# Performance work log

Measured on AMD Instinct MI355X. Metric: run time of the kernel, lower is better.

The kernel has to match this reference:

```python
import math
import jax, jax.numpy as jnp
import numpy as np

NUM_BUCKETS = 32
MAX_DISTANCE = 128
HEADS = 16
D_MODEL = 1024
SEQ = 1024
BATCH = 4
SCALE = (D_MODEL // HEADS) ** -0.5  # applied ONLY to the relative-position bias, per the source


def _rel_pos_bucket_causal(seq_len):
    """Causal T5 relative-position bucket: ret[i, j] for query i, key j."""
    pos = jnp.arange(seq_len)
    # rel_pos = k - q ; n = -rel_pos = q - k, clamped at 0 (causal branch)
    n = jnp.maximum(pos[:, None] - pos[None, :], 0)
    max_exact = NUM_BUCKETS // 2  # 16
    # log-spaced buckets for large distances; guard n>=1 to avoid log(0)
    val_large = max_exact + (
        jnp.log(jnp.maximum(n, 1).astype(jnp.float32) / max_exact)
        / math.log(MAX_DISTANCE / max_exact)
        * (NUM_BUCKETS - max_exact)
    ).astype(jnp.int32)
    val_large = jnp.minimum(val_large, NUM_BUCKETS - 1)
    return jnp.where(n < max_exact, n, val_large)  # [i, j] int32


def setup_inputs() -> dict:
    key = jax.random.key(0)
    ks = jax.random.split(key, 6)
    s = 0.02
    return {
        "x": jax.random.normal(ks[0], (BATCH, SEQ, D_MODEL), jnp.float32),
        "Wq": jax.random.normal(ks[1], (D_MODEL, D_MODEL), jnp.float32) * s,
        "bq": jnp.zeros((D_MODEL,), jnp.float32),
        "Wk": jax.random.normal(ks[2], (D_MODEL, D_MODEL), jnp.float32) * s,
        "bk": jnp.zeros((D_MODEL,), jnp.float32),
        "Wv": jax.random.normal(ks[3], (D_MODEL, D_MODEL), jnp.float32) * s,
        "bv": jnp.zeros((D_MODEL,), jnp.float32),
        "Wo": jax.random.normal(ks[4], (D_MODEL, D_MODEL), jnp.float32) * s,
        "bo": jnp.zeros((D_MODEL,), jnp.float32),
        "rel_emb": jax.random.normal(ks[5], (NUM_BUCKETS, HEADS), jnp.float32) * s,
    }


def reference(x, Wq, bq, Wk, bk, Wv, bv, Wo, bo, rel_emb):
    b, n, d = x.shape
    h, hd = HEADS, d // HEADS
    # projections (torch Linear: x @ W^T + b)
    q = (x @ Wq.T + bq).reshape(b, n, h, hd).transpose(0, 2, 1, 3)  # bhnd
    k = (x @ Wk.T + bk).reshape(b, n, h, hd).transpose(0, 2, 1, 3)
    v = (x @ Wv.T + bv).reshape(b, n, h, hd).transpose(0, 2, 1, 3)
    # unscaled dot-product scores (module does not scale q.k)
    sim = jnp.einsum("bhid,bhjd->bhij", q, k)
    # T5 relative-position bias, scaled by head_dim^-0.5
    rp_bucket = _rel_pos_bucket_causal(n)            # [i, j]
    bias = rel_emb[rp_bucket]                        # [i, j, h]
    sim = sim + jnp.transpose(bias, (2, 0, 1)) * SCALE  # broadcast over batch
    # additive causal mask (-inf above diagonal)
    i = jnp.arange(n)
    causal = jnp.where(i[None, :] > i[:, None], -jnp.inf, 0.0).astype(sim.dtype)
    sim = sim + causal
    attn = jax.nn.softmax(sim, axis=-1)
    out = jnp.einsum("bhij,bhjd->bhid", attn, v)
    out = out.transpose(0, 2, 1, 3).reshape(b, n, d)
    return out @ Wo.T + bo
```

## Files before the change

### kernel.cpp

```cpp
#include <hip/hip_runtime.h>
#include <hip/hip_bf16.h>
#include <stdint.h>

#define B_   4
#define SEQ_ 1024
#define DM   1024
#define H_   16
#define HD   64

typedef __bf16 bf16;
typedef __bf16 bf16x8 __attribute__((ext_vector_type(8)));
typedef __bf16 bf16x4v __attribute__((ext_vector_type(4)));
typedef __bf16 bf16x2 __attribute__((ext_vector_type(2)));
typedef float  f32x4 __attribute__((ext_vector_type(4)));

__device__ __forceinline__ void gl_lds16(const void* g, void* s_uniform) {
    __builtin_amdgcn_global_load_lds(
        (const __attribute__((address_space(1))) uint32_t*)g,
        (__attribute__((address_space(3))) uint32_t*)s_uniform,
        16, 0, 0);
}

__global__ __launch_bounds__(256) void prep_kernel(
    const float* __restrict__ x, const float* __restrict__ Wq,
    const float* __restrict__ Wk, const float* __restrict__ Wv,
    const float* __restrict__ Wo, const float* __restrict__ rel,
    bf16* __restrict__ xb, bf16* __restrict__ wqkvb, bf16* __restrict__ wob,
    float* __restrict__ biasT)
{
    int tid = blockIdx.x * 256 + threadIdx.x;
    int stride = gridDim.x * 256;

    for (int i = tid; i < (B_*SEQ_*DM)/4; i += stride) {
        float4 v = ((const float4*)x)[i];
        bf16x4v o; o[0]=(bf16)v.x; o[1]=(bf16)v.y; o[2]=(bf16)v.z; o[3]=(bf16)v.w;
        ((bf16x4v*)xb)[i] = o;
    }
    for (int i = tid; i < (3*DM*DM)/4; i += stride) {
        int n = i >> 8, k4 = i & 255;
        const float* src = (n < 1024) ? Wq : (n < 2048) ? Wk : Wv;
        float4 v = ((const float4*)(src + (size_t)(n & 1023) * DM))[k4];
        bf16x4v o; o[0]=(bf16)v.x; o[1]=(bf16)v.y; o[2]=(bf16)v.z; o[3]=(bf16)v.w;
        ((bf16x4v*)wqkvb)[i] = o;
    }
    for (int i = tid; i < (DM*DM)/4; i += stride) {
        float4 v = ((const float4*)Wo)[i];
        bf16x4v o; o[0]=(bf16)v.x; o[1]=(bf16)v.y; o[2]=(bf16)v.z; o[3]=(bf16)v.w;
        ((bf16x4v*)wob)[i] = o;
    }
    for (int i = tid; i < H_ * SEQ_; i += stride) {
        int h = i >> 10, dist = i & 1023;
        int bkt;
        if (dist < 16) {
            bkt = dist;
        } else {
            float r = logf((float)dist * (1.0f/16.0f)) / logf(8.0f) * 16.0f;
            int vb = 16 + (int)r;
            bkt = vb > 31 ? 31 : vb;
        }
        biasT[i] = rel[bkt * H_ + h] * 0.125f;
    }
}

template<int NT>
__global__ __launch_bounds__(256, 3) void gemm_ring(
    const bf16* __restrict__ Ag, const bf16* __restrict__ Bg,
    bf16* __restrict__ qb, bf16* __restrict__ kb, bf16* __restrict__ vtb,
    const float* __restrict__ bq, const float* __restrict__ bk,
    const float* __restrict__ bv)
{
    __shared__ __align__(16) bf16 tile[3][256 * 32];

    const int t = threadIdx.x;
    const int lane = t & 63, w = t >> 6;
    const int wr = w >> 1, wc = w & 1;
    const int row_l = lane & 15;
    const int lg = lane >> 4;

    int xcd = blockIdx.x & 7;
    int idx = blockIdx.x >> 3;
    int ty = (xcd >> 1) * 8 + idx / 12;
    int tx = (xcd & 1) * 12 + idx % 12;
    const int m0 = ty * 128, n0 = tx * 128;

    f32x4 acc[4][4] = {};

    auto STAGE = [&](int buf, int kt) {
        bf16* dst = &tile[buf][0];
        #pragma unroll
        for (int i = 0; i < 4; ++i) {
            int e = i * 2048 + t * 8;
            int r = e >> 5;
            int csw = ((t & 3) ^ (r & 3)) << 3;
            const bf16* src = (r < 128)
                ? (Ag + (long)(m0 + r) * 1024 + kt * 32 + csw)
                : (Bg + (long)(n0 + r - 128) * 1024 + kt * 32 + csw);
            gl_lds16(src, dst + i * 2048 + w * 512);
        }
    };

    auto COMPUTE = [&](int buf) {
        const bf16* bp = &tile[buf][0];
        bf16x8 af[4], bfr[4];
        #pragma unroll
        for (int m = 0; m < 4; ++m) {
            int ra = wr * 64 + m * 16 + row_l;
            af[m] = *(const bf16x8*)&bp[ra * 32 + ((lg ^ (ra & 3)) << 3)];
        }
        #pragma unroll
        for (int n = 0; n < 4; ++n) {
            int rb = 128 + wc * 64 + n * 16 + row_l;
            bfr[n] = *(const bf16x8*)&bp[rb * 32 + ((lg ^ (rb & 3)) << 3)];
        }
        #pragma unroll
        for (int m = 0; m < 4; ++m)
            #pragma unroll
            for (int n = 0; n < 4; ++n)
                acc[m][n] = __builtin_amdgcn_mfma_f32_16x16x32_bf16(
                    af[m], bfr[n], acc[m][n], 0, 0, 0);
    };

    STAGE(0, 0); STAGE(1, 1);
    asm volatile("s_waitcnt vmcnt(4)" ::: "memory");
    __builtin_amdgcn_s_barrier();

    int cb = 0;
    for (int kt = 0; kt < NT; ++kt) {
        int sb = cb - 1; if (sb < 0) sb += 3;
        if (kt + 2 < NT) STAGE(sb, kt + 2);
        COMPUTE(cb);
        if (kt + 2 < NT) { asm volatile("s_waitcnt vmcnt(4)" ::: "memory"); }
        else             { asm volatile("s_waitcnt vmcnt(0)" ::: "memory"); }
        __builtin_amdgcn_s_barrier();
        cb = (cb + 1 == 3) ? 0 : cb + 1;
    }

    const int rbase = (lane >> 4) * 4;

    if (n0 < 2048) {
        #pragma unroll
        for (int m = 0; m < 4; ++m) {
            #pragma unroll
            for (int n = 0; n < 4; ++n) {
                #pragma unroll
                for (int g = 0; g < 4; ++g) {
                    int gm = m0 + wr * 64 + m * 16 + rbase + g;
                    int gn = n0 + wc * 64 + n * 16 + row_l;
                    int which = gn >> 10, nn = gn & 1023;
                    int h = nn >> 6, d = nn & 63;
                    int b = gm >> 10, s = gm & 1023;
                    float v = acc[m][n][g] + ((which == 0) ? bq[nn] : bk[nn]);
                    bf16 bv16 = (bf16)v;
                    if (which == 0)
                        qb[((long)(b*H_ + h)*SEQ_ + s)*HD + d] = bv16;
                    else
                        kb[((long)(b*H_ + h)*SEQ_ + s)*HD + d] = bv16;
                }
            }
        }
    } else {
        bf16* lt = &tile[0][0];
        #pragma unroll
        for (int m = 0; m < 4; ++m) {
            #pragma unroll
            for (int n = 0; n < 4; ++n) {
                int nl = wc * 64 + n * 16 + row_l;
                int mlb = wr * 64 + m * 16 + rbase;
                float bvv = bv[(n0 & 1023) + nl];
                #pragma unroll
                for (int g2 = 0; g2 < 2; ++g2) {
                    bf16x2 pk;
                    pk[0] = (bf16)(acc[m][n][2*g2]     + bvv);
                    pk[1] = (bf16)(acc[m][n][2*g2 + 1] + bvv);
                    int ml = mlb + 2 * g2;
                    int byte = nl * 256 + ((ml * 2) ^ ((nl & 15) << 4));
                    *(bf16x2*)((char*)lt + byte) = pk;
                }
            }
        }
        __syncthreads();
        {
            int nl = t >> 1, sc = t & 1;
            int nn = (n0 & 1023) + nl;
            int h = nn >> 6, d = nn & 63;
            int b = m0 >> 10, s0 = (m0 & 1023) + sc * 64;
            bf16* dst = vtb + ((long)(b*H_ + h)*HD + d)*SEQ_ + s0;
            #pragma unroll
            for (int i = 0; i < 8; ++i) {
                int byte = nl * 256 + ((sc * 128 + i * 16) ^ ((nl & 15) << 4));
                *(float4*)(dst + i * 8) = *(const float4*)((char*)lt + byte);
            }
        }
    }
}

template<int NT>
__global__ __launch_bounds__(256, 2) void gemm_ring_o(
    const bf16* __restrict__ Ag, const bf16* __restrict__ Bg,
    float* __restrict__ outp, const float* __restrict__ bo)
{
    __shared__ __align__(16) bf16 tile[3][192 * 32];

    const int t = threadIdx.x;
    const int lane = t & 63, w = t >> 6;
    const int wr = w >> 1, wc = w & 1;
    const int row_l = lane & 15;
    const int lg = lane >> 4;

    int xcd = blockIdx.x & 7;
    int idx = blockIdx.x >> 3;
    int ty = (xcd >> 1) * 8 + (idx >> 3);
    int tx = (xcd & 1) * 8 + (idx & 7);
    const int m0 = ty * 128, n0 = tx * 64;

    f32x4 acc[4][2] = {};

    auto STAGE = [&](int buf, int kt) {
        bf16* dst = &tile[buf][0];
        #pragma unroll
        for (int i = 0; i < 3; ++i) {
            int e = i * 2048 + t * 8;
            int r = e >> 5;
            int csw = ((t & 3) ^ (r & 3)) << 3;
            const bf16* src = (r < 128)
                ? (Ag + (long)(m0 + r) * 1024 + kt * 32 + csw)
                : (Bg + (long)(n0 + r - 128) * 1024 + kt * 32 + csw);
            gl_lds16(src, dst + i * 2048 + w * 512);
        }
    };

    auto COMPUTE = [&](int buf) {
        const bf16* bp = &tile[buf][0];
        bf16x8 af[4], bfr[2];
        #pragma unroll
        for (int m = 0; m < 4; ++m) {
            int ra = wr * 64 + m * 16 + row_l;
            af[m] = *(const bf16x8*)&bp[ra * 32 + ((lg ^ (ra & 3)) << 3)];
        }
        #pragma unroll
        for (int n = 0; n < 2; ++n) {
            int rb = 128 + wc * 32 + n * 16 + row_l;
            bfr[n] = *(const bf16x8*)&bp[rb * 32 + ((lg ^ (rb & 3)) << 3)];
        }
        #pragma unroll
        for (int m = 0; m < 4; ++m)
            #pragma unroll
            for (int n = 0; n < 2; ++n)
                acc[m][n] = __builtin_amdgcn_mfma_f32_16x16x32_bf16(
                    af[m], bfr[n], acc[m][n], 0, 0, 0);
    };

    STAGE(0, 0); STAGE(1, 1);
    asm volatile("s_waitcnt vmcnt(3)" ::: "memory");
    __builtin_amdgcn_s_barrier();

    int cb = 0;
    for (int kt = 0; kt < NT; ++kt) {
        int sb = cb - 1; if (sb < 0) sb += 3;
        if (kt + 2 < NT) STAGE(sb, kt + 2);
        COMPUTE(cb);
        if (kt + 2 < NT) { asm volatile("s_waitcnt vmcnt(3)" ::: "memory"); }
        else             { asm volatile("s_waitcnt vmcnt(0)" ::: "memory"); }
        __builtin_amdgcn_s_barrier();
        cb = (cb + 1 == 3) ? 0 : cb + 1;
    }

    const int rbase = (lane >> 4) * 4;
    #pragma unroll
    for (int m = 0; m < 4; ++m) {
        #pragma unroll
        for (int n = 0; n < 2; ++n) {
            #pragma unroll
            for (int g = 0; g < 4; ++g) {
                int gm = m0 + wr * 64 + m * 16 + rbase + g;
                int gn = n0 + wc * 32 + n * 16 + row_l;
                outp[(long)gm * DM + gn] = acc[m][n][g] + bo[gn];
            }
        }
    }
}

#define PSTRIDE 72

__global__ __launch_bounds__(256, 4) void attn_kernel(
    const bf16* __restrict__ Qb, const bf16* __restrict__ Kb,
    const bf16* __restrict__ Vtb, const float* __restrict__ biasT,
    bf16* __restrict__ AO)
{
    __shared__ __align__(16) bf16 Ks[2][64 * 64];
    __shared__ __align__(16) bf16 Ps[4][16 * PSTRIDE];
    __shared__ float biasS[SEQ_];

    int t = threadIdx.x;
    int lane = t & 63, w = t >> 6;

    int bid = blockIdx.x;
    int xcd = bid & 7;
    int widx = bid >> 3;
    int rnd = widx >> 5;
    int lo  = widx & 31;
    int g = xcd * 8 + (lo >> 2);
    int a = lo & 3;
    int qt = (rnd == 0) ? a : (rnd == 1) ? 15 - a : (rnd == 2) ? 7 - a : 8 + a;
    int h = g & 15, b = g >> 4;

    int row_l = lane & 15;
    int ksl = (lane >> 4) * 8;
    int rbase = (lane >> 4) * 4;

    ((float4*)biasS)[t] = ((const float4*)(biasT + (long)h * SEQ_))[t];

    const bf16* Kbase = Kb + (long)g * SEQ_ * HD;
    const bf16* Vbase = Vtb + (long)g * HD * SEQ_;

    const bf16* Qp = Qb + ((long)g * SEQ_ + qt * 64 + w * 16) * HD;
    bf16x8 qf0 = *(const bf16x8*)&Qp[row_l * HD + ksl];
    bf16x8 qf1 = *(const bf16x8*)&Qp[row_l * HD + 32 + ksl];

    f32x4 oacc[4] = {};
    float lsum[4] = {0.f, 0.f, 0.f, 0.f};
    int ir[4];
    #pragma unroll
    for (int q = 0; q < 4; ++q) ir[q] = qt * 64 + w * 16 + rbase + q;

    auto stageK = [&](int jt) {
        bf16* dst = &Ks[jt & 1][0];
        #pragma unroll
        for (int i = 0; i < 2; ++i) {
            int e = i * 2048 + t * 8;
            int r = e >> 6;
            int csw = ((((e >> 3) & 7) ^ (r & 7)) << 3);
            gl_lds16(Kbase + (long)(jt * 64 + r) * HD + csw,
                     dst + i * 2048 + w * 512);
        }
    };

    stageK(0);

    for (int jt = 0; jt <= qt; ++jt) {
        asm volatile("s_waitcnt vmcnt(0)" ::: "memory");
        __builtin_amdgcn_s_barrier();

        if (jt < qt) stageK(jt + 1);

        bf16x8 vfr[4][2];
        #pragma unroll
        for (int f = 0; f < 4; ++f) {
            const bf16* vp = Vbase + (long)(f * 16 + row_l) * SEQ_ + jt * 64 + ksl;
            vfr[f][0] = *(const bf16x8*)vp;
            vfr[f][1] = *(const bf16x8*)(vp + 32);
        }

        f32x4 s[4] = {};
        __builtin_amdgcn_s_setprio(1);
        #pragma unroll
        for (int f = 0; f < 4; ++f) {
            int ra = f * 16 + row_l;
            int a0 = (ra * 64 + ksl)      ^ ((ra & 7) << 3);
            int a1 = (ra * 64 + 32 + ksl) ^ ((ra & 7) << 3);
            bf16x8 kf0 = *(const bf16x8*)&Ks[jt & 1][a0];
            bf16x8 kf1 = *(const bf16x8*)&Ks[jt & 1][a1];
            s[f] = __builtin_amdgcn_mfma_f32_16x16x32_bf16(qf0, kf0, s[f], 0,0,0);
            s[f] = __builtin_amdgcn_mfma_f32_16x16x32_bf16(qf1, kf1, s[f], 0,0,0);
        }
        __builtin_amdgcn_s_setprio(0);

        #pragma unroll
        for (int f = 0; f < 4; ++f) {
            int j = jt * 64 + f * 16 + row_l;
            #pragma unroll
            for (int q = 0; q < 4; ++q) {
                float sv = (j <= ir[q]) ? (s[f][q] + biasS[ir[q] - j]) : -1e30f;
                float p = __expf(sv);
                lsum[q] += p;
                Ps[w][(rbase + q) * PSTRIDE + f * 16 + row_l] = (bf16)p;
            }
        }
        bf16x8 pf0 = *(const bf16x8*)&Ps[w][row_l * PSTRIDE + ksl];
        bf16x8 pf1 = *(const bf16x8*)&Ps[w][row_l * PSTRIDE + 32 + ksl];

        __builtin_amdgcn_s_setprio(1);
        #pragma unroll
        for (int db = 0; db < 4; ++db) {
            oacc[db] = __builtin_amdgcn_mfma_f32_16x16x32_bf16(pf0, vfr[db][0], oacc[db], 0,0,0);
            oacc[db] = __builtin_amdgcn_mfma_f32_16x16x32_bf16(pf1, vfr[db][1], oacc[db], 0,0,0);
        }
        __builtin_amdgcn_s_setprio(0);
    }

    #pragma unroll
    for (int q = 0; q < 4; ++q) {
        float l = lsum[q];
        #pragma unroll
        for (int off = 1; off < 16; off <<= 1) l += __shfl_xor(l, off);
        float inv = 1.0f / l;
        long base = ((long)(b * SEQ_ + ir[q])) * DM + h * HD;
        #pragma unroll
        for (int db = 0; db < 4; ++db)
            AO[base + db * 16 + row_l] = (bf16)(oacc[db][q] * inv);
    }
}

extern "C" void kernel_launch(void* const* d_in, const int* in_sizes, int n_in,
                              void* d_out, int out_size, void* d_ws, size_t ws_size,
                              hipStream_t stream)
{
    const float* x   = (const float*)d_in[0];
    const float* Wq  = (const float*)d_in[1];
    const float* bq  = (const float*)d_in[2];
    const float* Wk  = (const float*)d_in[3];
    const float* bk  = (const float*)d_in[4];
    const float* Wv  = (const float*)d_in[5];
    const float* bv  = (const float*)d_in[6];
    const float* Wo  = (const float*)d_in[7];
    const float* bo  = (const float*)d_in[8];
    const float* rel = (const float*)d_in[9];
    float* out = (float*)d_out;

    char* ws = (char*)d_ws;
    bf16* xb    = (bf16*)ws;  ws += (size_t)B_*SEQ_*DM * 2;
    bf16* wqkvb = (bf16*)ws;  ws += (size_t)3*DM*DM * 2;
    bf16* wob   = (bf16*)ws;  ws += (size_t)DM*DM * 2;
    float* biasT= (float*)ws; ws += (size_t)H_*SEQ_ * 4;
    bf16* Qb    = (bf16*)ws;  ws += (size_t)B_*H_*SEQ_*HD * 2;
    bf16* Kb2   = (bf16*)ws;  ws += (size_t)B_*H_*SEQ_*HD * 2;
    bf16* Vtb   = (bf16*)ws;  ws += (size_t)B_*H_*SEQ_*HD * 2;
    bf16* AO    = (bf16*)ws;  ws += (size_t)B_*SEQ_*DM * 2;

    prep_kernel<<<2048, 256, 0, stream>>>(x, Wq, Wk, Wv, Wo, rel,
                                          xb, wqkvb, wob, biasT);

    gemm_ring<32><<<768, 256, 0, stream>>>(
        xb, wqkvb, Qb, Kb2, Vtb, bq, bk, bv);

    attn_kernel<<<1024, 256, 0, stream>>>(Qb, Kb2, Vtb, biasT, AO);

    gemm_ring_o<32><<<512, 256, 0, stream>>>(AO, wob, out, bo);
}
```

Before: 110.7 us.

## Pair causal q-tiles per 512-thread block sharing LDS-staged K/V

Attention blocks now have 8 waves covering two query tiles, p and 15-p, so every block does the same amount of causal work. K and V tiles are staged once into LDS with swizzling and shared by both tiles, replacing per-wave global V loads. Q and the bias are prescaled by log2(e) so the softmax can use exp2f. The cost is that waves on the short tile sit idle through barriers for the rest of the loop, and the larger block raises LDS and register pressure.

```diff
diff --git a/kernel.cpp b/kernel.cpp
--- a/kernel.cpp
+++ b/kernel.cpp
@@ -58,7 +58,7 @@
             int vb = 16 + (int)r;
             bkt = vb > 31 ? 31 : vb;
         }
-        biasT[i] = rel[bkt * H_ + h] * 0.125f;
+        biasT[i] = rel[bkt * H_ + h] * (0.125f * 1.4426950408889634f);
     }
 }
 
@@ -150,6 +150,7 @@
                     int h = nn >> 6, d = nn & 63;
                     int b = gm >> 10, s = gm & 1023;
                     float v = acc[m][n][g] + ((which == 0) ? bq[nn] : bk[nn]);
+                    if (which == 0) v *= 1.4426950408889634f;
                     bf16 bv16 = (bf16)v;
                     if (which == 0)
                         qb[((long)(b*H_ + h)*SEQ_ + s)*HD + d] = bv16;
@@ -282,13 +283,14 @@
 
 #define PSTRIDE 72
 
-__global__ __launch_bounds__(256, 4) void attn_kernel(
+__global__ __launch_bounds__(512, 4) void attn_kernel(
     const bf16* __restrict__ Qb, const bf16* __restrict__ Kb,
     const bf16* __restrict__ Vtb, const float* __restrict__ biasT,
     bf16* __restrict__ AO)
 {
     __shared__ __align__(16) bf16 Ks[2][64 * 64];
-    __shared__ __align__(16) bf16 Ps[4][16 * PSTRIDE];
+    __shared__ __align__(16) bf16 Vs[2][64 * 64];
+    __shared__ __align__(16) bf16 Ps[8][16 * PSTRIDE];
     __shared__ float biasS[SEQ_];
 
     int t = threadIdx.x;
@@ -296,24 +298,35 @@
 
     int bid = blockIdx.x;
     int xcd = bid & 7;
-    int widx = bid >> 3;
-    int rnd = widx >> 5;
-    int lo  = widx & 31;
-    int g = xcd * 8 + (lo >> 2);
-    int a = lo & 3;
-    int qt = (rnd == 0) ? a : (rnd == 1) ? 15 - a : (rnd == 2) ? 7 - a : 8 + a;
+    int rest = bid >> 3;
+    int g = xcd * 8 + (rest & 7);
+    int p = rest >> 3;
+    int qt_hi = 15 - p;
     int h = g & 15, b = g >> 4;
+
+    int qtw = (w < 4) ? p : qt_hi;
+    int row0 = qtw * 64 + (w & 3) * 16;
 
     int row_l = lane & 15;
     int ksl = (lane >> 4) * 8;
     int rbase = (lane >> 4) * 4;
 
-    ((float4*)biasS)[t] = ((const float4*)(biasT + (long)h * SEQ_))[t];
-
     const bf16* Kbase = Kb + (long)g * SEQ_ * HD;
     const bf16* Vbase = Vtb + (long)g * HD * SEQ_;
 
-    const bf16* Qp = Qb + ((long)g * SEQ_ + qt * 64 + w * 16) * HD;
+    auto stageKV = [&](int jt) {
+        int e = t * 8;
+        int r = e >> 6;
+        int csw = ((((e >> 3) & 7) ^ (r & 7)) << 3);
+        gl_lds16(Kbase + (long)(jt * 64 + r) * HD + csw, &Ks[jt & 1][0] + w * 512);
+        gl_lds16(Vbase + (long)r * SEQ_ + jt * 64 + csw, &Vs[jt & 1][0] + w * 512);
+    };
+
+    stageKV(0);
+    if (t < 256)
+        ((float4*)biasS)[t] = ((const float4*)(biasT + (long)h * SEQ_))[t];
+
+    const bf16* Qp = Qb + ((long)g * SEQ_ + row0) * HD;
     bf16x8 qf0 = *(const bf16x8*)&Qp[row_l * HD + ksl];
     bf16x8 qf1 = *(const bf16x8*)&Qp[row_l * HD + 32 + ksl];
 
@@ -321,71 +334,58 @@
     float lsum[4] = {0.f, 0.f, 0.f, 0.f};
     int ir[4];
     #pragma unroll
-    for (int q = 0; q < 4; ++q) ir[q] = qt * 64 + w * 16 + rbase + q;
-
-    auto stageK = [&](int jt) {
-        bf16* dst = &Ks[jt & 1][0];
-        #pragma unroll
-        for (int i = 0; i < 2; ++i) {
-            int e = i * 2048 + t * 8;
-            int r = e >> 6;
-            int csw = ((((e >> 3) & 7) ^ (r & 7)) << 3);
-            gl_lds16(Kbase + (long)(jt * 64 + r) * HD + csw,
-                     dst + i * 2048 + w * 512);
-        }
-    };
-
-    stageK(0);
-
-    for (int jt = 0; jt <= qt; ++jt) {
+    for (int q = 0; q < 4; ++q) ir[q] = row0 + rbase + q;
+
+    for (int jt = 0; jt <= qt_hi; ++jt) {
         asm volatile("s_waitcnt vmcnt(0)" ::: "memory");
         __builtin_amdgcn_s_barrier();
-
-        if (jt < qt) stageK(jt + 1);
-
-        bf16x8 vfr[4][2];
-        #pragma unroll
-        for (int f = 0; f < 4; ++f) {
-            const bf16* vp = Vbase + (long)(f * 16 + row_l) * SEQ_ + jt * 64 + ksl;
-            vfr[f][0] = *(const bf16x8*)vp;
-            vfr[f][1] = *(const bf16x8*)(vp + 32);
-        }
-
-        f32x4 s[4] = {};
-        __builtin_amdgcn_s_setprio(1);
-        #pragma unroll
-        for (int f = 0; f < 4; ++f) {
-            int ra = f * 16 + row_l;
-            int a0 = (ra * 64 + ksl)      ^ ((ra & 7) << 3);
-            int a1 = (ra * 64 + 32 + ksl) ^ ((ra & 7) << 3);
-            bf16x8 kf0 = *(const bf16x8*)&Ks[jt & 1][a0];
-            bf16x8 kf1 = *(const bf16x8*)&Ks[jt & 1][a1];
-            s[f] = __builtin_amdgcn_mfma_f32_16x16x32_bf16(qf0, kf0, s[f], 0,0,0);
-            s[f] = __builtin_amdgcn_mfma_f32_16x16x32_bf16(qf1, kf1, s[f], 0,0,0);
-        }
-        __builtin_amdgcn_s_setprio(0);
-
-        #pragma unroll
-        for (int f = 0; f < 4; ++f) {
-            int j = jt * 64 + f * 16 + row_l;
-            #pragma unroll
-            for (int q = 0; q < 4; ++q) {
-                float sv = (j <= ir[q]) ? (s[f][q] + biasS[ir[q] - j]) : -1e30f;
-                float p = __expf(sv);
-                lsum[q] += p;
-                Ps[w][(rbase + q) * PSTRIDE + f * 16 + row_l] = (bf16)p;
-            }
-        }
-        bf16x8 pf0 = *(const bf16x8*)&Ps[w][row_l * PSTRIDE + ksl];
-        bf16x8 pf1 = *(const bf16x8*)&Ps[w][row_l * PSTRIDE + 32 + ksl];
-
-        __builtin_amdgcn_s_setprio(1);
-        #pragma unroll
-        for (int db = 0; db < 4; ++db) {
-            oacc[db] = __builtin_amdgcn_mfma_f32_16x16x32_bf16(pf0, vfr[db][0], oacc[db], 0,0,0);
-            oacc[db] = __builtin_amdgcn_mfma_f32_16x16x32_bf16(pf1, vfr[db][1], oacc[db], 0,0,0);
-        }
-        __builtin_amdgcn_s_setprio(0);
+        if (jt < qt_hi) stageKV(jt + 1);
+
+        if (jt <= qtw) {
+            const bf16* kb_ = &Ks[jt & 1][0];
+            const bf16* vb_ = &Vs[jt & 1][0];
+
+            f32x4 s[4] = {};
+            __builtin_amdgcn_s_setprio(1);
+            #pragma unroll
+            for (int f = 0; f < 4; ++f) {
+                int ra = f * 16 + row_l;
+                int a0 = (ra * 64 + ksl)      ^ ((ra & 7) << 3);
+                int a1 = (ra * 64 + 32 + ksl) ^ ((ra & 7) << 3);
+                bf16x8 kf0 = *(const bf16x8*)&kb_[a0];
+                bf16x8 kf1 = *(const bf16x8*)&kb_[a1];
+                s[f] = __builtin_amdgcn_mfma_f32_16x16x32_bf16(qf0, kf0, s[f], 0,0,0);
+                s[f] = __builtin_amdgcn_mfma_f32_16x16x32_bf16(qf1, kf1, s[f], 0,0,0);
+            }
+            __builtin_amdgcn_s_setprio(0);
+
+            #pragma unroll
+            for (int f = 0; f < 4; ++f) {
+                int j = jt * 64 + f * 16 + row_l;
+                #pragma unroll
+                for (int q = 0; q < 4; ++q) {
+                    float sv = (j <= ir[q]) ? (s[f][q] + biasS[ir[q] - j]) : -1e30f;
+                    float pexp = exp2f(sv);
+                    lsum[q] += pexp;
+                    Ps[w][(rbase + q) * PSTRIDE + f * 16 + row_l] = (bf16)pexp;
+                }
+            }
+            bf16x8 pf0 = *(const bf16x8*)&Ps[w][row_l * PSTRIDE + ksl];
+            bf16x8 pf1 = *(const bf16x8*)&Ps[w][row_l * PSTRIDE + 32 + ksl];
+
+            __builtin_amdgcn_s_setprio(1);
+            #pragma unroll
+            for (int db = 0; db < 4; ++db) {
+                int ra = db * 16 + row_l;
+                int a0 = (ra * 64 + ksl)      ^ ((ra & 7) << 3);
+                int a1 = (ra * 64 + 32 + ksl) ^ ((ra & 7) << 3);
+                bf16x8 vf0 = *(const bf16x8*)&vb_[a0];
+                bf16x8 vf1 = *(const bf16x8*)&vb_[a1];
+                oacc[db] = __builtin_amdgcn_mfma_f32_16x16x32_bf16(pf0, vf0, oacc[db], 0,0,0);
+                oacc[db] = __builtin_amdgcn_mfma_f32_16x16x32_bf16(pf1, vf1, oacc[db], 0,0,0);
+            }
+            __builtin_amdgcn_s_setprio(0);
+        }
     }
 
     #pragma unroll
@@ -433,7 +433,7 @@
     gemm_ring<32><<<768, 256, 0, stream>>>(
         xb, wqkvb, Qb, Kb2, Vtb, bq, bk, bv);
 
-    attn_kernel<<<1024, 256, 0, stream>>>(Qb, Kb2, Vtb, biasT, AO);
+    attn_kernel<<<512, 512, 0, stream>>>(Qb, Kb2, Vtb, biasT, AO);
 
     gemm_ring_o<32><<<512, 256, 0, stream>>>(AO, wob, out, bo);
 }
```

New measurement: 98.83 us. 1.12x faster.
